# Optimization experiments

Measured on AMD Instinct MI355X. Metric: run time of the kernel, lower is better.

## Reference

```python
import jax, jax.numpy as jnp
import numpy as np

N = 100000      # nodes
E = 1600000     # edges (before self-loops)
F_IN = 128      # num_features
C = 32          # embedding_dim / output_dim per head
H = 4           # heads
SLOPE = 0.2     # PyG GATv2Conv default negative_slope


def setup_inputs() -> dict:
    key = jax.random.key(0)
    ks = jax.random.split(key, 16)
    def w(k, shp, fan):
        return jax.random.normal(k, shp, jnp.float32) / np.float32(np.sqrt(fan))
    return {
        "x": jax.random.normal(ks[0], (N, F_IN), jnp.float32),
        "edge_index": jax.random.randint(ks[1], (2, E), 0, N, jnp.int32),
        "W1l": w(ks[2], (F_IN, H * C), F_IN),
        "W1r": w(ks[3], (F_IN, H * C), F_IN),
        "att1": w(ks[4], (H, C), C),
        "b1": jnp.zeros((H * C,), jnp.float32),
        "W2l": w(ks[5], (H * C, H * C), H * C),
        "W2r": w(ks[6], (H * C, H * C), H * C),
        "att2": w(ks[7], (H, C), C),
        "b2": jnp.zeros((H * C,), jnp.float32),
        "W3l": w(ks[8], (H * C, H * C), H * C),
        "W3r": w(ks[9], (H * C, H * C), H * C),
        "att3": w(ks[10], (H, C), C),
        "b3": jnp.zeros((C,), jnp.float32),
    }


def gatv2_conv(x, src, dst, Wl, Wr, att, b, concat):
    """GATv2Conv: gather -> LeakyReLU attention -> segment softmax -> scatter-add."""
    n = x.shape[0]
    h, c = att.shape
    xl = (x @ Wl).reshape(n, h, c)   # source-side projection
    xr = (x @ Wr).reshape(n, h, c)   # target-side projection
    e = jax.nn.leaky_relu(xl[src] + xr[dst], SLOPE)          # [E, H, C]
    logits = jnp.einsum('ehc,hc->eh', e, att)                # [E, H]
    m = jax.ops.segment_max(logits, dst, num_segments=n)     # per-dst max
    ex = jnp.exp(logits - m[dst])
    den = jax.ops.segment_sum(ex, dst, num_segments=n)
    alpha = ex / den[dst]                                    # [E, H]
    out = jax.ops.segment_sum(alpha[:, :, None] * xl[src], dst, num_segments=n)  # [N,H,C]
    out = out.reshape(n, h * c) if concat else out.mean(axis=1)
    return out + b


def reference(x, edge_index, W1l, W1r, att1, b1, W2l, W2r, att2, b2, W3l, W3r, att3, b3):
    n = x.shape[0]
    loops = jnp.arange(n, dtype=edge_index.dtype)            # PyG adds self-loops
    src = jnp.concatenate([edge_index[0], loops])
    dst = jnp.concatenate([edge_index[1], loops])
    h = jax.nn.relu(gatv2_conv(x, src, dst, W1l, W1r, att1, b1, True))
    h = jax.nn.relu(gatv2_conv(h, src, dst, W2l, W2r, att2, b2, True))
    h = jax.nn.relu(gatv2_conv(h, src, dst, W3l, W3r, att3, b3, False))
    return h
```

## Files before the change

kernel.cpp:

```cpp
#include <hip/hip_runtime.h>
#include <hip/hip_bf16.h>
#include <hip/hip_fp16.h>

#define SLOPE 0.2f

typedef __attribute__((ext_vector_type(8))) short bf16x8;
typedef __attribute__((ext_vector_type(4))) float f32x4;
typedef __attribute__((ext_vector_type(2))) float f32x2;

__device__ __forceinline__ unsigned short bf16_rn(float f) {
    unsigned u = __float_as_uint(f);
    return (unsigned short)((u + 0x7FFFu + ((u >> 16) & 1u)) >> 16);
}
__device__ __forceinline__ float bf16_to_f32(unsigned short s) {
    return __uint_as_float(((unsigned)s) << 16);
}


__global__ __launch_bounds__(256) void fat_pa(const float* __restrict__ W0, const float* __restrict__ W1,
                                              const float* __restrict__ W2, const float* __restrict__ W3,
                                              const float* __restrict__ W4, const float* __restrict__ W5,
                                              unsigned short* __restrict__ Wtab,
                                              const int* __restrict__ srcv, const int* __restrict__ dstv,
                                              int* __restrict__ bcnt, int2* __restrict__ edge2,
                                              int E, int NB, int CAP) {
    __shared__ int lcnt[512];
    __shared__ int lbase[512];
    int b = blockIdx.x, t = threadIdx.x;
    if (b < 384) {
        int j = b >> 6;
        int e = ((b & 63) << 8) + t;
        const float* W = (j == 0) ? W0 : (j == 1) ? W1 : (j == 2) ? W2
                       : (j == 3) ? W3 : (j == 4) ? W4 : W5;
        int L = j >> 1, side = j & 1;
        unsigned short* hiT = Wtab + (size_t)L * 65536 + side * 16384;
        unsigned short* loT = hiT + 32768;
        int n = e >> 7, k = e & 127;
        float x = W[k * 128 + n];
        unsigned short h = bf16_rn(x);
        hiT[e] = h;
        loT[e] = bf16_rn(x - bf16_to_f32(h));
    } else {
        int base = (b - 384) * 16384;
        for (int i = t; i < 512; i += 256) lcnt[i] = 0;
        __syncthreads();
        #pragma unroll 4
        for (int j = 0; j < 64; ++j) {
            int idx = base + j * 256 + t;
            if (idx < E) atomicAdd(&lcnt[dstv[idx] >> 8], 1);
        }
        __syncthreads();
        for (int i = t; i < NB; i += 256) {
            int c = lcnt[i];
            lbase[i] = c ? atomicAdd(&bcnt[i], c) : 0;
            lcnt[i] = 0;
        }
        __syncthreads();
        #pragma unroll 4
        for (int j = 0; j < 64; ++j) {
            int idx = base + j * 256 + t;
            if (idx < E) {
                int s = srcv[idx], d = dstv[idx];
                int bk = d >> 8;
                int off = atomicAdd(&lcnt[bk], 1) + lbase[bk];
                if (off < CAP) edge2[(size_t)bk * CAP + off] = make_int2(s, d);
            }
        }
    }
}


__global__ __launch_bounds__(256) void k_scan(const int* __restrict__ in, int* __restrict__ out,
                                              int* bsums, int n) {
    __shared__ int wsum[4];
    int t = threadIdx.x;
    int base = blockIdx.x * 1024 + t * 4;
    int v0 = (base + 0 < n) ? in[base + 0] : 0;
    int v1 = (base + 1 < n) ? in[base + 1] : 0;
    int v2 = (base + 2 < n) ? in[base + 2] : 0;
    int v3 = (base + 3 < n) ? in[base + 3] : 0;
    int tsum = v0 + v1 + v2 + v3;
    int lane = t & 63, wid = t >> 6;
    int x = tsum;
    #pragma unroll
    for (int d = 1; d < 64; d <<= 1) {
        int y = __shfl_up(x, d);
        if (lane >= d) x += y;
    }
    if (lane == 63) wsum[wid] = x;
    __syncthreads();
    if (t == 0) {
        int a = 0;
        for (int w = 0; w < 4; ++w) { int b = wsum[w]; wsum[w] = a; a += b; }
    }
    __syncthreads();
    int excl = x - tsum + wsum[wid];
    if (base + 0 < n) out[base + 0] = excl;
    if (base + 1 < n) out[base + 1] = excl + v0;
    if (base + 2 < n) out[base + 2] = excl + v0 + v1;
    if (base + 3 < n) out[base + 3] = excl + v0 + v1 + v2;
    if (bsums != nullptr && t == 255) bsums[blockIdx.x] = excl + tsum;
}


__device__ __forceinline__ void binB_block(const int* __restrict__ gbase, const int* __restrict__ bcnt,
                                           const int2* __restrict__ edge2,
                                           int* __restrict__ rowptr, int* __restrict__ col,
                                           int N, int E, int NB, int CAP,
                                           unsigned char* ldsraw, int t, int bk) {
    int* cnt  = (int*)ldsraw;
    int* curs = (int*)(ldsraw + 1024);
    int* wsum = (int*)(ldsraw + 2048);
    cnt[t] = 0;
    __syncthreads();
    int m = bcnt[bk]; if (m > CAP) m = CAP;
    const int2* eb = edge2 + (size_t)bk * CAP;
    for (int e = t; e < m; e += 256) atomicAdd(&cnt[eb[e].y & 255], 1);
    __syncthreads();
    int v = cnt[t];
    int lane = t & 63, wid = t >> 6;
    int x = v;
    #pragma unroll
    for (int d = 1; d < 64; d <<= 1) {
        int y = __shfl_up(x, d);
        if (lane >= d) x += y;
    }
    if (lane == 63) wsum[wid] = x;
    __syncthreads();
    if (t == 0) {
        int a = 0;
        for (int w = 0; w < 4; ++w) { int b = wsum[w]; wsum[w] = a; a += b; }
    }
    __syncthreads();
    int excl = x - v + wsum[wid];
    int base = gbase[bk];
    int dst = (bk << 8) + t;
    if (dst < N) rowptr[dst] = base + excl;
    curs[t] = base + excl;
    if (bk == NB - 1 && t == 0) rowptr[N] = E;
    __syncthreads();
    for (int e = t; e < m; e += 256) {
        int2 ed = eb[e];
        int pos = atomicAdd(&curs[ed.y & 255], 1);
        col[pos] = ed.x;
    }
}


#define LDS_A_HI 0
#define LDS_A_LO 10240
#define LDS_B_HI 20480
#define LDS_B_LO 30720

__device__ __forceinline__ void gemm_block(const float* __restrict__ X,
                                           const unsigned short* __restrict__ WL,
                                           __half* __restrict__ Y0, __half* __restrict__ Y1,
                                           int M, int tile, int ysel,
                                           unsigned char* lds, int t) {
    const unsigned short* whi = WL + ysel * 16384;
    const unsigned short* wlo = whi + 32768;
    int row0 = tile * 128;
    int lane = t & 63, w = t >> 6;
    int ml = lane & 15, q = lane >> 4;
    int sm = t >> 1, sh = t & 1;
    int srow = row0 + sm;
    bool svalid = srow < M;

    f32x4 acc[2][8];
    #pragma unroll
    for (int i = 0; i < 2; ++i)
        #pragma unroll
        for (int j = 0; j < 8; ++j) acc[i][j] = (f32x4){0.f, 0.f, 0.f, 0.f};

    for (int ks = 0; ks < 4; ++ks) {
        int k0 = ks * 32;
        {
            float v[16];
            if (svalid) {
                const float* src = X + (size_t)srow * 128 + k0 + sh * 16;
                *(float4*)&v[0]  = *(const float4*)&src[0];
                *(float4*)&v[4]  = *(const float4*)&src[4];
                *(float4*)&v[8]  = *(const float4*)&src[8];
                *(float4*)&v[12] = *(const float4*)&src[12];
            } else {
                #pragma unroll
                for (int j = 0; j < 16; ++j) v[j] = 0.f;
            }
            unsigned hw[8], lw[8];
            #pragma unroll
            for (int j = 0; j < 8; ++j) {
                unsigned short h0 = bf16_rn(v[2 * j]);
                unsigned short h1 = bf16_rn(v[2 * j + 1]);
                unsigned short l0 = bf16_rn(v[2 * j] - bf16_to_f32(h0));
                unsigned short l1 = bf16_rn(v[2 * j + 1] - bf16_to_f32(h1));
                hw[j] = (unsigned)h0 | ((unsigned)h1 << 16);
                lw[j] = (unsigned)l0 | ((unsigned)l1 << 16);
            }
            unsigned char* pa = lds + LDS_A_HI + sm * 80 + sh * 32;
            *(uint4*)(pa)      = *(uint4*)&hw[0];
            *(uint4*)(pa + 16) = *(uint4*)&hw[4];
            unsigned char* pl = lds + LDS_A_LO + sm * 80 + sh * 32;
            *(uint4*)(pl)      = *(uint4*)&lw[0];
            *(uint4*)(pl + 16) = *(uint4*)&lw[4];
        }
        {
            #pragma unroll
            for (int cc = 0; cc < 2; ++cc) {
                int c = t + cc * 256;
                int n = c >> 2, kc = (c & 3) * 8;
                *(uint4*)(lds + LDS_B_HI + n * 80 + (c & 3) * 16) =
                    *(const uint4*)(whi + n * 128 + k0 + kc);
                *(uint4*)(lds + LDS_B_LO + n * 80 + (c & 3) * 16) =
                    *(const uint4*)(wlo + n * 128 + k0 + kc);
            }
        }
        __syncthreads();
        bf16x8 ah[2], al[2];
        #pragma unroll
        for (int mt = 0; mt < 2; ++mt) {
            int am = w * 32 + mt * 16 + ml;
            ah[mt] = *(const bf16x8*)(lds + LDS_A_HI + am * 80 + q * 16);
            al[mt] = *(const bf16x8*)(lds + LDS_A_LO + am * 80 + q * 16);
        }
        #pragma unroll
        for (int nt = 0; nt < 8; ++nt) {
            int bn = nt * 16 + ml;
            bf16x8 bh = *(const bf16x8*)(lds + LDS_B_HI + bn * 80 + q * 16);
            bf16x8 bl = *(const bf16x8*)(lds + LDS_B_LO + bn * 80 + q * 16);
            #pragma unroll
            for (int mt = 0; mt < 2; ++mt) {
                acc[mt][nt] = __builtin_amdgcn_mfma_f32_16x16x32_bf16(ah[mt], bh, acc[mt][nt], 0, 0, 0);
                acc[mt][nt] = __builtin_amdgcn_mfma_f32_16x16x32_bf16(ah[mt], bl, acc[mt][nt], 0, 0, 0);
                acc[mt][nt] = __builtin_amdgcn_mfma_f32_16x16x32_bf16(al[mt], bh, acc[mt][nt], 0, 0, 0);
            }
        }
        __syncthreads();
    }

    __half* Y = ysel ? Y1 : Y0;
    #pragma unroll
    for (int mt = 0; mt < 2; ++mt) {
        int rbase = row0 + w * 32 + mt * 16 + q * 4;
        #pragma unroll
        for (int r = 0; r < 4; ++r) {
            int row = rbase + r;
            if (row < M) {
                #pragma unroll
                for (int nt = 0; nt < 8; ++nt)
                    Y[(size_t)row * 128 + nt * 16 + ml] = __float2half(acc[mt][nt][r]);
            }
        }
    }
}

__global__ __launch_bounds__(256) void k_gemm(const float* __restrict__ X,
                                              const unsigned short* __restrict__ WL,
                                              __half* __restrict__ Y0, __half* __restrict__ Y1, int M) {
    __shared__ __align__(16) unsigned char lds[40960];
    gemm_block(X, WL, Y0, Y1, M, blockIdx.x, blockIdx.y, lds, threadIdx.x);
}


__global__ __launch_bounds__(256) void fat_g1(const float* __restrict__ X,
                                              const unsigned short* __restrict__ WL,
                                              __half* __restrict__ Y0, __half* __restrict__ Y1, int M,
                                              const int* __restrict__ gbase, const int* __restrict__ bcnt,
                                              const int2* __restrict__ edge2,
                                              int* __restrict__ rowptr, int* __restrict__ col,
                                              int N, int E, int NB, int CAP) {
    __shared__ __align__(16) unsigned char lds[40960];
    int b = blockIdx.x;
    if (b < NB) {
        binB_block(gbase, bcnt, edge2, rowptr, col, N, E, NB, CAP, lds, threadIdx.x, b);
    } else {
        int g = b - NB;
        int tiles = (M + 127) >> 7;
        gemm_block(X, WL, Y0, Y1, M, g % tiles, g / tiles, lds, threadIdx.x);
    }
}


__device__ __forceinline__ float quadsum(float t) {
    t += __int_as_float(__builtin_amdgcn_update_dpp(0, __float_as_int(t), 0xB1, 0xf, 0xf, true));
    t += __int_as_float(__builtin_amdgcn_update_dpp(0, __float_as_int(t), 0x4E, 0xf, 0xf, true));
    return t;
}

__device__ __forceinline__ void cvt8(const uint4& r, f32x2* x) {
    union { uint4 u; __half2 h[4]; } cv;
    cv.u = r;
    #pragma unroll
    for (int q = 0; q < 4; ++q) {
        float2 f = __half22float2(cv.h[q]);
        x[q] = (f32x2){f.x, f.y};
    }
}

template <bool MEAN>
__global__ __launch_bounds__(256) void fused_gat(const __half* __restrict__ XLh,
                                                 const __half* __restrict__ XRh,
                                                 const float* __restrict__ att,
                                                 const float* __restrict__ bias,
                                                 const int* __restrict__ rowptr,
                                                 const int* __restrict__ col,
                                                 float* __restrict__ OUT, int N) {
    int wave = (blockIdx.x * blockDim.x + threadIdx.x) >> 6;
    int lane = threadIdx.x & 63;
    int g = lane >> 4, sub = lane & 15;
    int dst = wave * 4 + g;
    bool vd = dst < N;
    int d0 = vd ? dst : 0;

    int start = vd ? rowptr[d0] : 0;
    int end   = vd ? rowptr[d0 + 1] : 0;

    f32x2 xr2[4], av2[4];
    {
        uint4 rxr = *(const uint4*)&XRh[(size_t)d0 * 128 + sub * 8];
        cvt8(rxr, xr2);
        float av[8];
        *(float4*)&av[0] = *(const float4*)&att[sub * 8];
        *(float4*)&av[4] = *(const float4*)&att[sub * 8 + 4];
        #pragma unroll
        for (int q = 0; q < 4; ++q) av2[q] = (f32x2){av[2 * q], av[2 * q + 1]};
    }

    int deg = end - start;
    int md = max(deg, __shfl_xor(deg, 16));
    md = max(md, __shfl_xor(md, 32));

    f32x2 acc2[4];
    float s;
    {
        uint4 r = *(const uint4*)&XLh[(size_t)d0 * 128 + sub * 8];
        f32x2 xs[4];
        cvt8(r, xs);
        f32x2 d2 = (f32x2){0.f, 0.f};
        #pragma unroll
        for (int q = 0; q < 4; ++q) {
            f32x2 u = xs[q] + xr2[q];
            f32x2 lu = u * SLOPE;
            u.x = fmaxf(u.x, lu.x);
            u.y = fmaxf(u.y, lu.y);
            d2 += u * av2[q];
        }
        float tS = quadsum(d2.x + d2.y);
        float wS = __expf(fminf(tS, 80.f));
        s = wS;
        #pragma unroll
        for (int q = 0; q < 4; ++q) acc2[q] = xs[q] * wS;
    }

    for (int i = 0; i < md; i += 2) {
        int pA = start + i, pB = start + i + 1;
        bool vA = pA < end, vB = pB < end;
        int iA = col[vA ? pA : 0];
        int iB = col[vB ? pB : 0];
        uint4 rA = *(const uint4*)&XLh[(size_t)iA * 128 + sub * 8];
        uint4 rB = *(const uint4*)&XLh[(size_t)iB * 128 + sub * 8];
        f32x2 xA[4], xB[4];
        cvt8(rA, xA);
        cvt8(rB, xB);
        f32x2 dA2 = (f32x2){0.f, 0.f}, dB2 = (f32x2){0.f, 0.f};
        #pragma unroll
        for (int q = 0; q < 4; ++q) {
            f32x2 uA = xA[q] + xr2[q];
            f32x2 uB = xB[q] + xr2[q];
            f32x2 lA = uA * SLOPE;
            f32x2 lB = uB * SLOPE;
            uA.x = fmaxf(uA.x, lA.x); uA.y = fmaxf(uA.y, lA.y);
            uB.x = fmaxf(uB.x, lB.x); uB.y = fmaxf(uB.y, lB.y);
            dA2 += uA * av2[q];
            dB2 += uB * av2[q];
        }
        float tA = quadsum(dA2.x + dA2.y);
        float tB = quadsum(dB2.x + dB2.y);
        float wA = __expf(fminf(tA, 80.f));
        float wB = __expf(fminf(tB, 80.f));
        wA = vA ? wA : 0.f;
        wB = vB ? wB : 0.f;
        s += wA + wB;
        #pragma unroll
        for (int q = 0; q < 4; ++q) {
            acc2[q] += xA[q] * wA;
            acc2[q] += xB[q] * wB;
        }
    }

    float rs = 1.0f / s;
    if (MEAN) {
        float o[8];
        #pragma unroll
        for (int q = 0; q < 4; ++q) {
            float vx = acc2[q].x * rs, vy = acc2[q].y * rs;
            vx += __shfl_xor(vx, 4); vy += __shfl_xor(vy, 4);
            vx += __shfl_xor(vx, 8); vy += __shfl_xor(vy, 8);
            o[2 * q]     = fmaxf(fmaf(vx, 0.25f, bias[sub * 8 + 2 * q]), 0.f);
            o[2 * q + 1] = fmaxf(fmaf(vy, 0.25f, bias[sub * 8 + 2 * q + 1]), 0.f);
        }
        if (vd && sub < 4) {
            *(float4*)&OUT[(size_t)d0 * 32 + sub * 8]     = *(float4*)&o[0];
            *(float4*)&OUT[(size_t)d0 * 32 + sub * 8 + 4] = *(float4*)&o[4];
        }
    } else {
        float o[8];
        #pragma unroll
        for (int q = 0; q < 4; ++q) {
            o[2 * q]     = fmaxf(fmaf(acc2[q].x, rs, bias[sub * 8 + 2 * q]), 0.f);
            o[2 * q + 1] = fmaxf(fmaf(acc2[q].y, rs, bias[sub * 8 + 2 * q + 1]), 0.f);
        }
        if (vd) {
            *(float4*)&OUT[(size_t)d0 * 128 + sub * 8]     = *(float4*)&o[0];
            *(float4*)&OUT[(size_t)d0 * 128 + sub * 8 + 4] = *(float4*)&o[4];
        }
    }
}


extern "C" void kernel_launch(void* const* d_in, const int* in_sizes, int n_in,
                              void* d_out, int out_size, void* d_ws, size_t ws_size,
                              hipStream_t stream) {
    const float* x   = (const float*)d_in[0];
    const int*   ei  = (const int*)d_in[1];
    const float* W1l = (const float*)d_in[2];
    const float* W1r = (const float*)d_in[3];
    const float* at1 = (const float*)d_in[4];
    const float* b1  = (const float*)d_in[5];
    const float* W2l = (const float*)d_in[6];
    const float* W2r = (const float*)d_in[7];
    const float* at2 = (const float*)d_in[8];
    const float* b2  = (const float*)d_in[9];
    const float* W3l = (const float*)d_in[10];
    const float* W3r = (const float*)d_in[11];
    const float* at3 = (const float*)d_in[12];
    const float* b3  = (const float*)d_in[13];
    float* out = (float*)d_out;

    int N = in_sizes[0] / 128;
    int E = in_sizes[1] / 2;
    const int* srcv = ei;
    const int* dstv = ei + E;
    int NB = (N + 255) >> 8;

    int avg = E / NB;
    int sd = (int)(8.0 * __builtin_sqrt((double)avg)) + 64;
    int CAP = avg + sd;

    char* p = (char*)d_ws;
    auto alloc = [&](size_t bytes) -> void* {
        void* r = (void*)p;
        p += (bytes + 255) & ~(size_t)255;
        return r;
    };
    __half* XLh = (__half*)alloc((size_t)N * 128 * 2);
    __half* XRh = (__half*)alloc((size_t)N * 128 * 2);
    float*  H   = (float*)alloc((size_t)N * 128 * 4);
    int* rowptr = (int*)alloc((size_t)(N + 1) * 4);
    int* bcnt   = (int*)alloc((size_t)NB * 4);
    int* gbase  = (int*)alloc((size_t)NB * 4);
    int* col    = (int*)alloc((size_t)E * 4);
    int2* edge2 = (int2*)alloc((size_t)NB * CAP * 8);
    unsigned short* Wtab = (unsigned short*)alloc((size_t)6 * 65536 * 2);

    int tiles = (N + 127) / 128;
    int nfb = (N + 15) / 16;
    int ab = (E + 16383) / 16384;

    hipMemsetAsync(bcnt, 0, (size_t)NB * 4, stream);
    fat_pa<<<384 + ab, 256, 0, stream>>>(W1l, W1r, W2l, W2r, W3l, W3r, Wtab,
                                         srcv, dstv, bcnt, edge2, E, NB, CAP);
    k_scan<<<1, 256, 0, stream>>>(bcnt, gbase, nullptr, NB);
    fat_g1<<<NB + 2 * tiles, 256, 0, stream>>>(x, Wtab, XLh, XRh, N,
                                               gbase, bcnt, edge2, rowptr, col, N, E, NB, CAP);
    fused_gat<false><<<nfb, 256, 0, stream>>>(XLh, XRh, at1, b1, rowptr, col, H, N);
    k_gemm<<<dim3(tiles, 2), 256, 0, stream>>>(H, Wtab + 1 * 65536, XLh, XRh, N);
    fused_gat<false><<<nfb, 256, 0, stream>>>(XLh, XRh, at2, b2, rowptr, col, H, N);
    k_gemm<<<dim3(tiles, 2), 256, 0, stream>>>(H, Wtab + 2 * 65536, XLh, XRh, N);
    fused_gat<true><<<nfb, 256, 0, stream>>>(XLh, XRh, at3, b3, rowptr, col, out, N);
}
```

Measured before the change: 523.6 us.

## Replace global CSR scan with bucket-padded start/end pairs and smaller binning blocks

Drops the single-block scan kernel and the global rowptr by giving each 256-node bucket a fixed CAP-sized slot in col, so per-node ranges are stored as int2 (start,end). This removes one kernel launch and its serialization between binning and CSR build. The binning blocks also now process 4096 edges instead of 16384, quadrupling the number of blocks for more parallelism. The cost is a larger padded col array with gaps between buckets, and out-of-range padded edge loads now read col[start].

```diff
diff --git a/kernel.cpp b/kernel.cpp
--- a/kernel.cpp
+++ b/kernel.cpp
@@ -41,11 +41,11 @@
         hiT[e] = h;
         loT[e] = bf16_rn(x - bf16_to_f32(h));
     } else {
-        int base = (b - 384) * 16384;
+        int base = (b - 384) * 4096;
         for (int i = t; i < 512; i += 256) lcnt[i] = 0;
         __syncthreads();
         #pragma unroll 4
-        for (int j = 0; j < 64; ++j) {
+        for (int j = 0; j < 16; ++j) {
             int idx = base + j * 256 + t;
             if (idx < E) atomicAdd(&lcnt[dstv[idx] >> 8], 1);
         }
@@ -57,7 +57,7 @@
         }
         __syncthreads();
         #pragma unroll 4
-        for (int j = 0; j < 64; ++j) {
+        for (int j = 0; j < 16; ++j) {
             int idx = base + j * 256 + t;
             if (idx < E) {
                 int s = srcv[idx], d = dstv[idx];
@@ -70,43 +70,10 @@
 }
 
 
-__global__ __launch_bounds__(256) void k_scan(const int* __restrict__ in, int* __restrict__ out,
-                                              int* bsums, int n) {
-    __shared__ int wsum[4];
-    int t = threadIdx.x;
-    int base = blockIdx.x * 1024 + t * 4;
-    int v0 = (base + 0 < n) ? in[base + 0] : 0;
-    int v1 = (base + 1 < n) ? in[base + 1] : 0;
-    int v2 = (base + 2 < n) ? in[base + 2] : 0;
-    int v3 = (base + 3 < n) ? in[base + 3] : 0;
-    int tsum = v0 + v1 + v2 + v3;
-    int lane = t & 63, wid = t >> 6;
-    int x = tsum;
-    #pragma unroll
-    for (int d = 1; d < 64; d <<= 1) {
-        int y = __shfl_up(x, d);
-        if (lane >= d) x += y;
-    }
-    if (lane == 63) wsum[wid] = x;
-    __syncthreads();
-    if (t == 0) {
-        int a = 0;
-        for (int w = 0; w < 4; ++w) { int b = wsum[w]; wsum[w] = a; a += b; }
-    }
-    __syncthreads();
-    int excl = x - tsum + wsum[wid];
-    if (base + 0 < n) out[base + 0] = excl;
-    if (base + 1 < n) out[base + 1] = excl + v0;
-    if (base + 2 < n) out[base + 2] = excl + v0 + v1;
-    if (base + 3 < n) out[base + 3] = excl + v0 + v1 + v2;
-    if (bsums != nullptr && t == 255) bsums[blockIdx.x] = excl + tsum;
-}
-
-
-__device__ __forceinline__ void binB_block(const int* __restrict__ gbase, const int* __restrict__ bcnt,
+__device__ __forceinline__ void binB_block(const int* __restrict__ bcnt,
                                            const int2* __restrict__ edge2,
-                                           int* __restrict__ rowptr, int* __restrict__ col,
-                                           int N, int E, int NB, int CAP,
+                                           int2* __restrict__ rp, int* __restrict__ col,
+                                           int N, int NB, int CAP,
                                            unsigned char* ldsraw, int t, int bk) {
     int* cnt  = (int*)ldsraw;
     int* curs = (int*)(ldsraw + 1024);
@@ -133,11 +100,10 @@
     }
     __syncthreads();
     int excl = x - v + wsum[wid];
-    int base = gbase[bk];
+    int base = bk * CAP;
     int dst = (bk << 8) + t;
-    if (dst < N) rowptr[dst] = base + excl;
+    if (dst < N) rp[dst] = make_int2(base + excl, base + excl + v);
     curs[t] = base + excl;
-    if (bk == NB - 1 && t == 0) rowptr[N] = E;
     __syncthreads();
     for (int e = t; e < m; e += 256) {
         int2 ed = eb[e];
@@ -264,14 +230,14 @@
 __global__ __launch_bounds__(256) void fat_g1(const float* __restrict__ X,
                                               const unsigned short* __restrict__ WL,
                                               __half* __restrict__ Y0, __half* __restrict__ Y1, int M,
-                                              const int* __restrict__ gbase, const int* __restrict__ bcnt,
+                                              const int* __restrict__ bcnt,
                                               const int2* __restrict__ edge2,
-                                              int* __restrict__ rowptr, int* __restrict__ col,
-                                              int N, int E, int NB, int CAP) {
+                                              int2* __restrict__ rp, int* __restrict__ col,
+                                              int N, int NB, int CAP) {
     __shared__ __align__(16) unsigned char lds[40960];
     int b = blockIdx.x;
     if (b < NB) {
-        binB_block(gbase, bcnt, edge2, rowptr, col, N, E, NB, CAP, lds, threadIdx.x, b);
+        binB_block(bcnt, edge2, rp, col, N, NB, CAP, lds, threadIdx.x, b);
     } else {
         int g = b - NB;
         int tiles = (M + 127) >> 7;
@@ -301,7 +267,7 @@
                                                  const __half* __restrict__ XRh,
                                                  const float* __restrict__ att,
                                                  const float* __restrict__ bias,
-                                                 const int* __restrict__ rowptr,
+                                                 const int2* __restrict__ rp,
                                                  const int* __restrict__ col,
                                                  float* __restrict__ OUT, int N) {
     int wave = (blockIdx.x * blockDim.x + threadIdx.x) >> 6;
@@ -311,8 +277,8 @@
     bool vd = dst < N;
     int d0 = vd ? dst : 0;
 
-    int start = vd ? rowptr[d0] : 0;
-    int end   = vd ? rowptr[d0 + 1] : 0;
+    int2 se = vd ? rp[d0] : make_int2(0, 0);
+    int start = se.x, end = se.y;
 
     f32x2 xr2[4], av2[4];
     {
@@ -354,8 +320,8 @@
     for (int i = 0; i < md; i += 2) {
         int pA = start + i, pB = start + i + 1;
         bool vA = pA < end, vB = pB < end;
-        int iA = col[vA ? pA : 0];
-        int iB = col[vB ? pB : 0];
+        int iA = col[vA ? pA : start];
+        int iB = col[vB ? pB : start];
         uint4 rA = *(const uint4*)&XLh[(size_t)iA * 128 + sub * 8];
         uint4 rB = *(const uint4*)&XLh[(size_t)iB * 128 + sub * 8];
         f32x2 xA[4], xB[4];
@@ -455,26 +421,24 @@
     __half* XLh = (__half*)alloc((size_t)N * 128 * 2);
     __half* XRh = (__half*)alloc((size_t)N * 128 * 2);
     float*  H   = (float*)alloc((size_t)N * 128 * 4);
-    int* rowptr = (int*)alloc((size_t)(N + 1) * 4);
+    int2* rp    = (int2*)alloc((size_t)N * 8);
     int* bcnt   = (int*)alloc((size_t)NB * 4);
-    int* gbase  = (int*)alloc((size_t)NB * 4);
-    int* col    = (int*)alloc((size_t)E * 4);
+    int* col    = (int*)alloc((size_t)NB * CAP * 4);
     int2* edge2 = (int2*)alloc((size_t)NB * CAP * 8);
     unsigned short* Wtab = (unsigned short*)alloc((size_t)6 * 65536 * 2);
 
     int tiles = (N + 127) / 128;
     int nfb = (N + 15) / 16;
-    int ab = (E + 16383) / 16384;
+    int ab = (E + 4095) / 4096;
 
     hipMemsetAsync(bcnt, 0, (size_t)NB * 4, stream);
     fat_pa<<<384 + ab, 256, 0, stream>>>(W1l, W1r, W2l, W2r, W3l, W3r, Wtab,
                                          srcv, dstv, bcnt, edge2, E, NB, CAP);
-    k_scan<<<1, 256, 0, stream>>>(bcnt, gbase, nullptr, NB);
     fat_g1<<<NB + 2 * tiles, 256, 0, stream>>>(x, Wtab, XLh, XRh, N,
-                                               gbase, bcnt, edge2, rowptr, col, N, E, NB, CAP);
-    fused_gat<false><<<nfb, 256, 0, stream>>>(XLh, XRh, at1, b1, rowptr, col, H, N);
+                                               bcnt, edge2, rp, col, N, NB, CAP);
+    fused_gat<false><<<nfb, 256, 0, stream>>>(XLh, XRh, at1, b1, rp, col, H, N);
     k_gemm<<<dim3(tiles, 2), 256, 0, stream>>>(H, Wtab + 1 * 65536, XLh, XRh, N);
-    fused_gat<false><<<nfb, 256, 0, stream>>>(XLh, XRh, at2, b2, rowptr, col, H, N);
+    fused_gat<false><<<nfb, 256, 0, stream>>>(XLh, XRh, at2, b2, rp, col, H, N);
     k_gemm<<<dim3(tiles, 2), 256, 0, stream>>>(H, Wtab + 2 * 65536, XLh, XRh, N);
-    fused_gat<true><<<nfb, 256, 0, stream>>>(XLh, XRh, at3, b3, rowptr, col, out, N);
-}
+    fused_gat<true><<<nfb, 256, 0, stream>>>(XLh, XRh, at3, b3, rp, col, out, N);
+}
```

Measured after the change: 485.7 us. -7.2%, faster.
